# Kernel optimization log

Measured on AMD Instinct MI355X. Metric: run time of the kernel, lower is better.

Reference implementation:

```python
import jax, jax.numpy as jnp
import numpy as np

N, E, NREL = 50000, 800000, 4
IN, EMB, HID, OUT, LVL = 32, 32, 32, 32, 3


def setup_inputs() -> dict:
    key = jax.random.key(0)
    ks = jax.random.split(key, 24)
    f32 = jnp.float32
    inp = {
        'x': jax.random.normal(ks[0], (N, IN), f32),
        'node_feat': jax.random.normal(ks[1], (N, EMB), f32),
        'edge_feat': jax.random.normal(ks[2], (E, EMB), f32),
        'src': jax.random.randint(ks[3], (E,), 0, N, jnp.int32),
        'dst': jax.random.randint(ks[4], (E,), 0, N, jnp.int32),
        'eid': jax.random.randint(ks[5], (E,), 0, NREL, jnp.int32),
        # layer 1 (in_feat=IN)
        'Wr1': jax.random.normal(ks[6], (NREL, IN + 2 * EMB, HID), f32) * 0.1,
        'attn_w1': jax.random.normal(ks[7], (EMB + HID, 1), f32) * 0.1,
        'loop_w1': jax.random.normal(ks[8], (EMB, HID), f32) * 0.1,
        'h_bias1': jax.random.normal(ks[9], (HID,), f32) * 0.1,
        'amrm_W1': jax.random.normal(ks[10], (LVL, HID, HID), f32) * 0.1,
        'amrm_b1': jax.random.normal(ks[11], (LVL, HID), f32) * 0.1,
        'amrm_a1': jax.random.normal(ks[12], (HID, 1), f32) * 0.1,
        # layer 2 (in_feat=HID)
        'Wr2': jax.random.normal(ks[13], (NREL, HID + 2 * EMB, OUT), f32) * 0.1,
        'attn_w2': jax.random.normal(ks[14], (EMB + OUT, 1), f32) * 0.1,
        'loop_w2': jax.random.normal(ks[15], (EMB, OUT), f32) * 0.1,
        'h_bias2': jax.random.normal(ks[16], (OUT,), f32) * 0.1,
        'amrm_W2': jax.random.normal(ks[17], (LVL, OUT, OUT), f32) * 0.1,
        'amrm_b2': jax.random.normal(ks[18], (LVL, OUT), f32) * 0.1,
        'amrm_a2': jax.random.normal(ks[19], (OUT, 1), f32) * 0.1,
    }
    return inp


def _rp_layer(feat, node_feat, src, dst, eid, edge_feat,
              Wr, attn_w, loop_w, h_bias, amrm_W, amrm_b, amrm_a):
    n = node_feat.shape[0]
    ones_e = jnp.ones((src.shape[0],), feat.dtype)
    # symmetric-ish degree norm: feat scaled by out-degree^-1/2
    deg_out = jnp.clip(jax.ops.segment_sum(ones_e, src, num_segments=n), 1.0)
    feat = feat * (deg_out ** -0.5)[:, None]
    # per-edge gather + relation-typed linear (grouped GEMM over NREL types)
    xe = jnp.concatenate([feat[src], edge_feat, node_feat[dst]], axis=1)  # [E, in+2*emb]
    m = jnp.zeros((xe.shape[0], Wr.shape[2]), feat.dtype)
    for r in range(Wr.shape[0]):
        m = m + jnp.where((eid == r)[:, None], xe @ Wr[r], 0.0)
    # edge attention + segment softmax over incoming edges per dst node
    z = jax.nn.leaky_relu(jnp.concatenate([node_feat[dst], m], axis=1) @ attn_w)  # [E,1]
    zmax = jax.ops.segment_max(z, dst, num_segments=n)
    ez = jnp.exp(z - zmax[dst])
    a = ez / jax.ops.segment_sum(ez, dst, num_segments=n)[dst]
    # scatter-sum aggregation
    h = jax.ops.segment_sum(a * m, dst, num_segments=n)
    h = h + node_feat @ loop_w
    deg_in = jnp.clip(jax.ops.segment_sum(ones_e, dst, num_segments=n), 1.0)
    h = h * (deg_in ** -0.5)[:, None] + h_bias
    # adaptive multi-level relation module
    lv = jax.nn.relu(jnp.einsum('nh,lho->nlo', h, amrm_W) + amrm_b[None])  # [N,L,O]
    sc = jax.nn.softmax(jnp.einsum('nlo,o->nl', lv, amrm_a[:, 0]), axis=-1)  # [N,L]
    return jnp.einsum('nl,nlo->no', sc, lv)


def reference(x, node_feat, edge_feat, src, dst, eid,
              Wr1, attn_w1, loop_w1, h_bias1, amrm_W1, amrm_b1, amrm_a1,
              Wr2, attn_w2, loop_w2, h_bias2, amrm_W2, amrm_b2, amrm_a2):
    h = jax.nn.relu(_rp_layer(x, node_feat, src, dst, eid, edge_feat,
                              Wr1, attn_w1, loop_w1, h_bias1, amrm_W1, amrm_b1, amrm_a1))
    h = jax.nn.relu(_rp_layer(h, node_feat, src, dst, eid, edge_feat,
                              Wr2, attn_w2, loop_w2, h_bias2, amrm_W2, amrm_b2, amrm_a2))
    return h
```

## Files before the change

kernel.cpp:

```cpp
#include <hip/hip_runtime.h>

#define NN 50000
#define NE 800000

#define O_DEGIN   0
#define O_DEGOUT  50048
#define O_ROWPTR  100096
#define O_CURSOR  150208
#define O_EINFO   200256
#define O_FEATN   1800256
#define O_ZF      3400256
#define O_ZNRD    3600320
#define O_VV      3800384
#define O_EZ      3800832
#define O_NFT     4600832
#define O_WDENT   6200832
#define O_YACCT   6450880
#define O_H1      19250880
#define O_PACC    20850880


__global__ __launch_bounds__(256) void k_deg(const int* __restrict__ src,
                                             const int* __restrict__ dst,
                                             int* degin, int* degout) {
    int e = blockIdx.x * 256 + threadIdx.x;
    if (e < NE) {
        atomicAdd(&degin[dst[e]], 1);
        atomicAdd(&degout[src[e]], 1);
    }
}

__global__ __launch_bounds__(1024) void k_scan(const int* __restrict__ degin,
                                               int* rowptr, int* cursor) {
    __shared__ int swsum[16];
    __shared__ int stot;
    int t = threadIdx.x;
    int lane = t & 63, w = t >> 6;
    int carry = 0;
    for (int ch = 0; ch < 4; ch++) {
        int base = ch * 16384 + t * 16;
        int v[16];
        int s = 0;
#pragma unroll
        for (int j = 0; j < 16; j++) {
            v[j] = (base + j < NN) ? degin[base + j] : 0;
            s += v[j];
        }
        int incl = s;
#pragma unroll
        for (int off = 1; off < 64; off <<= 1) {
            int x = __shfl_up(incl, off, 64);
            if (lane >= off) incl += x;
        }
        if (lane == 63) swsum[w] = incl;
        __syncthreads();
        if (w == 0) {
            int y = (lane < 16) ? swsum[lane] : 0;
            int yi = y;
#pragma unroll
            for (int off = 1; off < 16; off <<= 1) {
                int x = __shfl_up(yi, off, 64);
                if (lane >= off) yi += x;
            }
            if (lane < 16) swsum[lane] = yi - y;
            if (lane == 15) stot = yi;
        }
        __syncthreads();
        int excl = carry + swsum[w] + (incl - s);
#pragma unroll
        for (int j = 0; j < 16; j++) {
            if (base + j < NN) { rowptr[base + j] = excl; cursor[base + j] = excl; }
            excl += v[j];
        }
        carry += stot;
        __syncthreads();
    }
    if (t == 0) rowptr[NN] = carry;
}

__global__ __launch_bounds__(256) void k_scatter(const int* __restrict__ src,
                                                 const int* __restrict__ dst,
                                                 const int* __restrict__ eid,
                                                 int* cursor, int2* einfo) {
    int e = blockIdx.x * 256 + threadIdx.x;
    if (e >= NE) return;
    int slot = atomicAdd(&cursor[dst[e]], 1);
    einfo[slot] = make_int2(src[e] | (eid[e] << 20), e);
}


__global__ __launch_bounds__(384) void k_prevec(const float* __restrict__ Wr,
                                                const float* __restrict__ attw,
                                                float* __restrict__ vvec) {
    int t = threadIdx.x;
    int r = (t >> 5) & 3, k = t & 31, part = t >> 7;
    int row = (part == 0) ? (32 + k) : (part == 1) ? k : (64 + k);
    const float* wrow = Wr + (size_t)r * 3072 + row * 32;
    float s = 0.f;
#pragma unroll
    for (int c = 0; c < 32; c++) s += wrow[c] * attw[32 + c];
    vvec[t] = s;
}

__global__ __launch_bounds__(128) void k_nodeproj(const float* __restrict__ feat,
                                                  const float* __restrict__ nfeat,
                                                  const float* __restrict__ attw,
                                                  const float* __restrict__ vvec,
                                                  const int* __restrict__ degout,
                                                  float* __restrict__ featn,
                                                  float* __restrict__ nfT,
                                                  float* __restrict__ zF,
                                                  float* __restrict__ znrd) {
    int n = blockIdx.x * 128 + threadIdx.x;
    if (n >= NN) return;
    int dg = degout[n];
    float sc0 = rsqrtf((float)(dg > 1 ? dg : 1));
    const float* fin = feat + (size_t)n * 32;
    const float* nin = nfeat + (size_t)n * 32;
    float fv[32], nv[32];
#pragma unroll
    for (int k = 0; k < 32; k += 4) {
        float4 f4 = *(const float4*)&fin[k];
        fv[k] = f4.x * sc0; fv[k + 1] = f4.y * sc0;
        fv[k + 2] = f4.z * sc0; fv[k + 3] = f4.w * sc0;
        float4 n4 = *(const float4*)&nin[k];
        nv[k] = n4.x; nv[k + 1] = n4.y; nv[k + 2] = n4.z; nv[k + 3] = n4.w;
    }
    float* fo = featn + (size_t)n * 32;
#pragma unroll
    for (int k = 0; k < 32; k += 4)
        *(float4*)&fo[k] = make_float4(fv[k], fv[k + 1], fv[k + 2], fv[k + 3]);
#pragma unroll
    for (int k = 0; k < 32; k++) nfT[(size_t)k * NN + n] = nv[k];
    float zn = 0.f;
#pragma unroll
    for (int k = 0; k < 32; k++) zn += nv[k] * attw[k];
#pragma unroll
    for (int r = 0; r < 4; r++) {
        float zf = 0.f, zd = 0.f;
        const float* vf = vvec + 128 + r * 32;
        const float* vd = vvec + 256 + r * 32;
#pragma unroll
        for (int k = 0; k < 32; k++) { zf += fv[k] * vf[k]; zd += nv[k] * vd[k]; }
        zF[r * NN + n] = zf;
        znrd[r * NN + n] = zn + zd;
    }
}

__global__ __launch_bounds__(256) void k_ez(const int* __restrict__ src,
                                            const int* __restrict__ dst,
                                            const int* __restrict__ eid,
                                            const float* __restrict__ efeat,
                                            const float* __restrict__ zF,
                                            const float* __restrict__ znrd,
                                            const float* __restrict__ vvec,
                                            float* __restrict__ ez) {
    int e = blockIdx.x * 256 + threadIdx.x;
    int s = src[e], d = dst[e], r = eid[e];
    const float* er = efeat + (size_t)e * 32;
    float d0 = 0.f, d1 = 0.f, d2 = 0.f, d3 = 0.f;
#pragma unroll
    for (int k = 0; k < 32; k += 4) {
        float4 f = *(const float4*)&er[k];
        d0 += f.x * vvec[k]       + f.y * vvec[k + 1]
            + f.z * vvec[k + 2]   + f.w * vvec[k + 3];
        d1 += f.x * vvec[32 + k]  + f.y * vvec[33 + k]
            + f.z * vvec[34 + k]  + f.w * vvec[35 + k];
        d2 += f.x * vvec[64 + k]  + f.y * vvec[65 + k]
            + f.z * vvec[66 + k]  + f.w * vvec[67 + k];
        d3 += f.x * vvec[96 + k]  + f.y * vvec[97 + k]
            + f.z * vvec[98 + k]  + f.w * vvec[99 + k];
    }
    float dot = (r == 0) ? d0 : (r == 1) ? d1 : (r == 2) ? d2 : d3;
    float z = znrd[r * NN + d] + zF[r * NN + s] + dot;
    z = z > 0.f ? z : 0.01f * z;
    ez[e] = __expf(z);
}

__global__ __launch_bounds__(512) void k_agg(const int* __restrict__ rowptr,
                                             const int2* __restrict__ einfo,
                                             const float* __restrict__ ez,
                                             const float* __restrict__ efeat,
                                             const float* __restrict__ featn,
                                             float* __restrict__ yaccT,
                                             float* __restrict__ wdenT) {
    __shared__ float sT[256 * 9];
    int tid = threadIdx.x;
    int lane = tid & 63;
    int wid = tid >> 6;
    int n0 = blockIdx.x * 8;
    int n = n0 + wid;
    int c = lane & 31;
    int p = lane >> 5;

    int rp0 = rowptr[n];
    int deg = rowptr[n + 1] - rp0;

    float yf0 = 0.f, yf1 = 0.f, yf2 = 0.f, yf3 = 0.f;
    float ye0 = 0.f, ye1 = 0.f, ye2 = 0.f, ye3 = 0.f;
    float w0 = 0.f, w1 = 0.f, w2 = 0.f, w3 = 0.f, den = 0.f;

    int2 meA = make_int2(0, 0), meB = make_int2(0, 0);
    float ezA = 0.f, efA = 0.f, fnA = 0.f;
    if (p < deg) {
        meA = einfo[rp0 + p];
        ezA = ez[meA.y];
        efA = efeat[(size_t)meA.y * 32 + c];
        fnA = featn[(size_t)(meA.x & 0xFFFFF) * 32 + c];
    }
    if (p + 2 < deg) meB = einfo[rp0 + p + 2];

    for (int t = p; t < deg; t += 2) {
        float ezB = 0.f, efB = 0.f, fnB = 0.f;
        int2 meC = make_int2(0, 0);
        if (t + 2 < deg) {
            ezB = ez[meB.y];
            efB = efeat[(size_t)meB.y * 32 + c];
            fnB = featn[(size_t)(meB.x & 0xFFFFF) * 32 + c];
        }
        if (t + 4 < deg) meC = einfo[rp0 + t + 4];
        int rb = meA.x >> 20;
        float e0 = (rb == 0) ? ezA : 0.f;
        float e1 = (rb == 1) ? ezA : 0.f;
        float e2 = (rb == 2) ? ezA : 0.f;
        float e3 = (rb == 3) ? ezA : 0.f;
        yf0 += e0 * fnA; yf1 += e1 * fnA; yf2 += e2 * fnA; yf3 += e3 * fnA;
        ye0 += e0 * efA; ye1 += e1 * efA; ye2 += e2 * efA; ye3 += e3 * efA;
        w0 += e0; w1 += e1; w2 += e2; w3 += e3;
        den += ezA;
        meA = meB; ezA = ezB; efA = efB; fnA = fnB; meB = meC;
    }

    yf0 += __shfl_xor(yf0, 32); yf1 += __shfl_xor(yf1, 32);
    yf2 += __shfl_xor(yf2, 32); yf3 += __shfl_xor(yf3, 32);
    ye0 += __shfl_xor(ye0, 32); ye1 += __shfl_xor(ye1, 32);
    ye2 += __shfl_xor(ye2, 32); ye3 += __shfl_xor(ye3, 32);
    w0 += __shfl_xor(w0, 32); w1 += __shfl_xor(w1, 32);
    w2 += __shfl_xor(w2, 32); w3 += __shfl_xor(w3, 32);
    den += __shfl_xor(den, 32);

    if (lane < 5) {
        float wv = (lane == 0) ? w0 : (lane == 1) ? w1 : (lane == 2) ? w2
                 : (lane == 3) ? w3 : den;
        wdenT[lane * NN + n] = wv;
    }

    {
        int kb = 128 * p + c;
        sT[(kb +  0) * 9 + wid] = p ? ye0 : yf0;
        sT[(kb + 32) * 9 + wid] = p ? ye1 : yf1;
        sT[(kb + 64) * 9 + wid] = p ? ye2 : yf2;
        sT[(kb + 96) * 9 + wid] = p ? ye3 : yf3;
    }
    __syncthreads();
    int k = tid >> 1, hf = tid & 1;
    float4 v = make_float4(sT[k * 9 + hf * 4 + 0], sT[k * 9 + hf * 4 + 1],
                           sT[k * 9 + hf * 4 + 2], sT[k * 9 + hf * 4 + 3]);
    *(float4*)&yaccT[(size_t)k * NN + n0 + hf * 4] = v;
}

__global__ __launch_bounds__(256) void k_postA(const float* __restrict__ yaccT,
                                               const float* __restrict__ wdenT,
                                               const float* __restrict__ nfT,
                                               const float* __restrict__ Wr,
                                               float* __restrict__ pacc) {
    int n = blockIdx.x * 256 + threadIdx.x;
    if (n >= NN) return;
    int r = blockIdx.y;

    float nv[32];
#pragma unroll
    for (int k = 0; k < 32; k++) nv[k] = nfT[(size_t)k * NN + n];
    float wr = wdenT[r * NN + n];

    const float* W = Wr + (size_t)r * 3072;
    const float* ufc = yaccT + (size_t)(r * 32) * NN + n;
    const float* uec = yaccT + (size_t)(128 + r * 32) * NN + n;

    float acc[32];
#pragma unroll
    for (int i = 0; i < 32; i++) acc[i] = 0.f;
    for (int k4 = 0; k4 < 32; k4 += 4) {
        float a0 = ufc[(size_t)(k4 + 0) * NN], a1 = ufc[(size_t)(k4 + 1) * NN];
        float a2 = ufc[(size_t)(k4 + 2) * NN], a3 = ufc[(size_t)(k4 + 3) * NN];
        float b0 = uec[(size_t)(k4 + 0) * NN], b1 = uec[(size_t)(k4 + 1) * NN];
        float b2 = uec[(size_t)(k4 + 2) * NN], b3 = uec[(size_t)(k4 + 3) * NN];
        float g0 = wr * nv[k4],     g1 = wr * nv[k4 + 1];
        float g2 = wr * nv[k4 + 2], g3 = wr * nv[k4 + 3];
        const float* Wk = W + k4 * 32;
#pragma unroll
        for (int i = 0; i < 32; i++)
            acc[i] += a0 * Wk[i]        + a1 * Wk[32 + i]
                    + a2 * Wk[64 + i]   + a3 * Wk[96 + i]
                    + b0 * Wk[1024 + i] + b1 * Wk[1056 + i]
                    + b2 * Wk[1088 + i] + b3 * Wk[1120 + i]
                    + g0 * Wk[2048 + i] + g1 * Wk[2080 + i]
                    + g2 * Wk[2112 + i] + g3 * Wk[2144 + i];
    }
    float* po = pacc + (size_t)(r * 32) * NN + n;
#pragma unroll
    for (int i = 0; i < 32; i++) po[(size_t)i * NN] = acc[i];
}

__global__ __launch_bounds__(256) void k_postB(const int* __restrict__ rowptr,
                                               const float* __restrict__ pacc,
                                               const float* __restrict__ wdenT,
                                               const float* __restrict__ nfT,
                                               const float* __restrict__ lw,
                                               const float* __restrict__ hbias,
                                               const float* __restrict__ aW,
                                               const float* __restrict__ ab,
                                               const float* __restrict__ aa,
                                               float* __restrict__ out) {
    int n = blockIdx.x * 256 + threadIdx.x;
    if (n >= NN) return;
    int deg = rowptr[n + 1] - rowptr[n];
    float den = wdenT[4 * NN + n];
    float invden = (deg > 0) ? 1.f / den : 0.f;

    float nv[32];
#pragma unroll
    for (int k = 0; k < 32; k++) nv[k] = nfT[(size_t)k * NN + n];

    float h[32];
#pragma unroll
    for (int i = 0; i < 32; i++) {
        float s = pacc[(size_t)i * NN + n]
                + pacc[(size_t)(32 + i) * NN + n]
                + pacc[(size_t)(64 + i) * NN + n]
                + pacc[(size_t)(96 + i) * NN + n];
        h[i] = s * invden;
    }
    for (int k4 = 0; k4 < 32; k4 += 4) {
        const float* Lk = lw + k4 * 32;
#pragma unroll
        for (int i = 0; i < 32; i++)
            h[i] += nv[k4] * Lk[i] + nv[k4 + 1] * Lk[32 + i]
                  + nv[k4 + 2] * Lk[64 + i] + nv[k4 + 3] * Lk[96 + i];
    }
    float hsc = rsqrtf((float)(deg > 1 ? deg : 1));
#pragma unroll
    for (int i = 0; i < 32; i++) h[i] = h[i] * hsc + hbias[i];

    float acc[32];
    float s[3];
#pragma unroll
    for (int l = 0; l < 3; l++) {
        const float* A = aW + (size_t)l * 1024;
#pragma unroll
        for (int i = 0; i < 32; i++) acc[i] = ab[l * 32 + i];
        for (int k4 = 0; k4 < 32; k4 += 4) {
            const float* Ak = A + k4 * 32;
#pragma unroll
            for (int i = 0; i < 32; i++)
                acc[i] += h[k4] * Ak[i] + h[k4 + 1] * Ak[32 + i]
                        + h[k4 + 2] * Ak[64 + i] + h[k4 + 3] * Ak[96 + i];
        }
        float sl = 0.f;
#pragma unroll
        for (int i = 0; i < 32; i++) {
            float lv = acc[i] > 0.f ? acc[i] : 0.f;
            sl += lv * aa[i];
        }
        s[l] = sl;
    }
    float mx = fmaxf(s[0], fmaxf(s[1], s[2]));
    float e0 = __expf(s[0] - mx), e1 = __expf(s[1] - mx), e2 = __expf(s[2] - mx);
    float inv = 1.f / (e0 + e1 + e2);
    float scl[3] = {e0 * inv, e1 * inv, e2 * inv};

    float outv[32];
#pragma unroll
    for (int i = 0; i < 32; i++) outv[i] = 0.f;
#pragma unroll
    for (int l = 0; l < 3; l++) {
        const float* A = aW + (size_t)l * 1024;
#pragma unroll
        for (int i = 0; i < 32; i++) acc[i] = ab[l * 32 + i];
        for (int k4 = 0; k4 < 32; k4 += 4) {
            const float* Ak = A + k4 * 32;
#pragma unroll
            for (int i = 0; i < 32; i++)
                acc[i] += h[k4] * Ak[i] + h[k4 + 1] * Ak[32 + i]
                        + h[k4 + 2] * Ak[64 + i] + h[k4 + 3] * Ak[96 + i];
        }
#pragma unroll
        for (int i = 0; i < 32; i++) {
            float lv = acc[i] > 0.f ? acc[i] : 0.f;
            outv[i] += scl[l] * lv;
        }
    }
    float* op = out + (size_t)n * 32;
#pragma unroll
    for (int i = 0; i < 32; i += 4)
        *(float4*)&op[i] = make_float4(fmaxf(outv[i], 0.f), fmaxf(outv[i + 1], 0.f),
                                       fmaxf(outv[i + 2], 0.f), fmaxf(outv[i + 3], 0.f));
}


static void launch_layer(const float* feat, const float* nf, const float* efeat,
                         const int* src, const int* dst, const int* eid,
                         const float* Wr, const float* attw, const float* lw,
                         const float* hb, const float* aW, const float* ab,
                         const float* aa, float* wsf, int* wsi, float* out,
                         hipStream_t stream) {
    k_prevec<<<1, 384, 0, stream>>>(Wr, attw, wsf + O_VV);
    k_nodeproj<<<391, 128, 0, stream>>>(feat, nf, attw, wsf + O_VV, wsi + O_DEGOUT,
                                        wsf + O_FEATN, wsf + O_NFT,
                                        wsf + O_ZF, wsf + O_ZNRD);
    k_ez<<<3125, 256, 0, stream>>>(src, dst, eid, efeat, wsf + O_ZF, wsf + O_ZNRD,
                                   wsf + O_VV, wsf + O_EZ);
    k_agg<<<6250, 512, 0, stream>>>(wsi + O_ROWPTR, (const int2*)(wsi + O_EINFO),
                                    wsf + O_EZ, efeat, wsf + O_FEATN,
                                    wsf + O_YACCT, wsf + O_WDENT);
    k_postA<<<dim3(196, 4), 256, 0, stream>>>(wsf + O_YACCT, wsf + O_WDENT,
                                              wsf + O_NFT, Wr, wsf + O_PACC);
    k_postB<<<196, 256, 0, stream>>>(wsi + O_ROWPTR, wsf + O_PACC, wsf + O_WDENT,
                                     wsf + O_NFT, lw, hb, aW, ab, aa, out);
}

extern "C" void kernel_launch(void* const* d_in, const int* in_sizes, int n_in,
                              void* d_out, int out_size, void* d_ws, size_t ws_size,
                              hipStream_t stream) {
    const float* x     = (const float*)d_in[0];
    const float* nfeat = (const float*)d_in[1];
    const float* efeat = (const float*)d_in[2];
    const int*   src   = (const int*)d_in[3];
    const int*   dst   = (const int*)d_in[4];
    const int*   eid   = (const int*)d_in[5];
    const float* Wr1   = (const float*)d_in[6];
    const float* attw1 = (const float*)d_in[7];
    const float* lw1   = (const float*)d_in[8];
    const float* hb1   = (const float*)d_in[9];
    const float* aW1   = (const float*)d_in[10];
    const float* ab1   = (const float*)d_in[11];
    const float* aa1   = (const float*)d_in[12];
    const float* Wr2   = (const float*)d_in[13];
    const float* attw2 = (const float*)d_in[14];
    const float* lw2   = (const float*)d_in[15];
    const float* hb2   = (const float*)d_in[16];
    const float* aW2   = (const float*)d_in[17];
    const float* ab2   = (const float*)d_in[18];
    const float* aa2   = (const float*)d_in[19];

    float* wsf = (float*)d_ws;
    int*   wsi = (int*)d_ws;
    float* out = (float*)d_out;

    hipMemsetAsync(d_ws, 0, (size_t)O_ROWPTR * 4, stream);

    k_deg<<<NE / 256, 256, 0, stream>>>(src, dst, wsi + O_DEGIN, wsi + O_DEGOUT);
    k_scan<<<1, 1024, 0, stream>>>(wsi + O_DEGIN, wsi + O_ROWPTR, wsi + O_CURSOR);
    k_scatter<<<NE / 256, 256, 0, stream>>>(src, dst, eid, wsi + O_CURSOR,
                                            (int2*)(wsi + O_EINFO));

    launch_layer(x, nfeat, efeat, src, dst, eid, Wr1, attw1, lw1, hb1, aW1, ab1, aa1,
                 wsf, wsi, wsf + O_H1, stream);
    launch_layer(wsf + O_H1, nfeat, efeat, src, dst, eid, Wr2, attw2, lw2, hb2,
                 aW2, ab2, aa2, wsf, wsi, out, stream);
}
```

Before: 700.8 us.

## Fuse relation-typed projection into edge aggregation kernel, drop transposed intermediates

Fuses the per-relation Wr projection (formerly k_postA) into the aggregation kernel. Each warp now multiplies its per-node accumulated sums by Wr from shared memory, and writes a node-major 32-wide result plus the softmax denominator. The edge loop now handles 4 edges in parallel per wave with float2 loads instead of 2 edges with scalar loads. This removes the large transposed yaccT/pacc round-trips through global memory and one kernel launch. The cost is extra per-block arithmetic and repeated Wr reads from cache in the aggregation kernel.

```diff
diff --git a/kernel.cpp b/kernel.cpp
--- a/kernel.cpp
+++ b/kernel.cpp
@@ -18,6 +18,7 @@
 #define O_YACCT   6450880
 #define O_H1      19250880
 #define O_PACC    20850880
+#define O_HACC    O_PACC
 
 
 __global__ __launch_bounds__(256) void k_deg(const int* __restrict__ src,
@@ -177,134 +178,119 @@
     ez[e] = __expf(z);
 }
 
-__global__ __launch_bounds__(512) void k_agg(const int* __restrict__ rowptr,
-                                             const int2* __restrict__ einfo,
-                                             const float* __restrict__ ez,
-                                             const float* __restrict__ efeat,
-                                             const float* __restrict__ featn,
-                                             float* __restrict__ yaccT,
-                                             float* __restrict__ wdenT) {
-    __shared__ float sT[256 * 9];
+#define R2(v) { v += __shfl_xor(v, 16); v += __shfl_xor(v, 32); }
+__global__ __launch_bounds__(512) void k_aggf(const int* __restrict__ rowptr,
+                                              const int2* __restrict__ einfo,
+                                              const float* __restrict__ ez,
+                                              const float* __restrict__ efeat,
+                                              const float* __restrict__ featn,
+                                              const float* __restrict__ nfeat,
+                                              const float* __restrict__ Wr,
+                                              float* __restrict__ hacc,
+                                              float* __restrict__ wden) {
+    __shared__ alignas(16) float sT[8 * 256];
+    __shared__ alignas(16) float snv[8 * 32];
+    __shared__ float sw[8 * 4];
     int tid = threadIdx.x;
     int lane = tid & 63;
     int wid = tid >> 6;
-    int n0 = blockIdx.x * 8;
-    int n = n0 + wid;
-    int c = lane & 31;
-    int p = lane >> 5;
+    int n = blockIdx.x * 8 + wid;
+    int g = lane >> 4;
+    int c2 = lane & 15;
+
+    if (lane < 32) snv[wid * 32 + lane] = nfeat[(size_t)n * 32 + lane];
 
     int rp0 = rowptr[n];
     int deg = rowptr[n + 1] - rp0;
 
-    float yf0 = 0.f, yf1 = 0.f, yf2 = 0.f, yf3 = 0.f;
-    float ye0 = 0.f, ye1 = 0.f, ye2 = 0.f, ye3 = 0.f;
+    float2 yf0 = {0.f, 0.f}, yf1 = {0.f, 0.f}, yf2 = {0.f, 0.f}, yf3 = {0.f, 0.f};
+    float2 ye0 = {0.f, 0.f}, ye1 = {0.f, 0.f}, ye2 = {0.f, 0.f}, ye3 = {0.f, 0.f};
     float w0 = 0.f, w1 = 0.f, w2 = 0.f, w3 = 0.f, den = 0.f;
 
     int2 meA = make_int2(0, 0), meB = make_int2(0, 0);
-    float ezA = 0.f, efA = 0.f, fnA = 0.f;
-    if (p < deg) {
-        meA = einfo[rp0 + p];
+    float ezA = 0.f; float2 efA = {0.f, 0.f}, fnA = {0.f, 0.f};
+    if (g < deg) {
+        meA = einfo[rp0 + g];
         ezA = ez[meA.y];
-        efA = efeat[(size_t)meA.y * 32 + c];
-        fnA = featn[(size_t)(meA.x & 0xFFFFF) * 32 + c];
-    }
-    if (p + 2 < deg) meB = einfo[rp0 + p + 2];
-
-    for (int t = p; t < deg; t += 2) {
-        float ezB = 0.f, efB = 0.f, fnB = 0.f;
+        efA = *(const float2*)&efeat[(size_t)meA.y * 32 + c2 * 2];
+        fnA = *(const float2*)&featn[(size_t)(meA.x & 0xFFFFF) * 32 + c2 * 2];
+    }
+    if (g + 4 < deg) meB = einfo[rp0 + g + 4];
+
+    for (int t = g; t < deg; t += 4) {
+        float ezB = 0.f; float2 efB = {0.f, 0.f}, fnB = {0.f, 0.f};
         int2 meC = make_int2(0, 0);
-        if (t + 2 < deg) {
+        if (t + 4 < deg) {
             ezB = ez[meB.y];
-            efB = efeat[(size_t)meB.y * 32 + c];
-            fnB = featn[(size_t)(meB.x & 0xFFFFF) * 32 + c];
-        }
-        if (t + 4 < deg) meC = einfo[rp0 + t + 4];
+            efB = *(const float2*)&efeat[(size_t)meB.y * 32 + c2 * 2];
+            fnB = *(const float2*)&featn[(size_t)(meB.x & 0xFFFFF) * 32 + c2 * 2];
+        }
+        if (t + 8 < deg) meC = einfo[rp0 + t + 8];
         int rb = meA.x >> 20;
         float e0 = (rb == 0) ? ezA : 0.f;
         float e1 = (rb == 1) ? ezA : 0.f;
         float e2 = (rb == 2) ? ezA : 0.f;
         float e3 = (rb == 3) ? ezA : 0.f;
-        yf0 += e0 * fnA; yf1 += e1 * fnA; yf2 += e2 * fnA; yf3 += e3 * fnA;
-        ye0 += e0 * efA; ye1 += e1 * efA; ye2 += e2 * efA; ye3 += e3 * efA;
+        yf0.x += e0 * fnA.x; yf0.y += e0 * fnA.y;
+        yf1.x += e1 * fnA.x; yf1.y += e1 * fnA.y;
+        yf2.x += e2 * fnA.x; yf2.y += e2 * fnA.y;
+        yf3.x += e3 * fnA.x; yf3.y += e3 * fnA.y;
+        ye0.x += e0 * efA.x; ye0.y += e0 * efA.y;
+        ye1.x += e1 * efA.x; ye1.y += e1 * efA.y;
+        ye2.x += e2 * efA.x; ye2.y += e2 * efA.y;
+        ye3.x += e3 * efA.x; ye3.y += e3 * efA.y;
         w0 += e0; w1 += e1; w2 += e2; w3 += e3;
         den += ezA;
         meA = meB; ezA = ezB; efA = efB; fnA = fnB; meB = meC;
     }
 
-    yf0 += __shfl_xor(yf0, 32); yf1 += __shfl_xor(yf1, 32);
-    yf2 += __shfl_xor(yf2, 32); yf3 += __shfl_xor(yf3, 32);
-    ye0 += __shfl_xor(ye0, 32); ye1 += __shfl_xor(ye1, 32);
-    ye2 += __shfl_xor(ye2, 32); ye3 += __shfl_xor(ye3, 32);
-    w0 += __shfl_xor(w0, 32); w1 += __shfl_xor(w1, 32);
-    w2 += __shfl_xor(w2, 32); w3 += __shfl_xor(w3, 32);
-    den += __shfl_xor(den, 32);
-
-    if (lane < 5) {
-        float wv = (lane == 0) ? w0 : (lane == 1) ? w1 : (lane == 2) ? w2
-                 : (lane == 3) ? w3 : den;
-        wdenT[lane * NN + n] = wv;
-    }
-
-    {
-        int kb = 128 * p + c;
-        sT[(kb +  0) * 9 + wid] = p ? ye0 : yf0;
-        sT[(kb + 32) * 9 + wid] = p ? ye1 : yf1;
-        sT[(kb + 64) * 9 + wid] = p ? ye2 : yf2;
-        sT[(kb + 96) * 9 + wid] = p ? ye3 : yf3;
-    }
-    __syncthreads();
-    int k = tid >> 1, hf = tid & 1;
-    float4 v = make_float4(sT[k * 9 + hf * 4 + 0], sT[k * 9 + hf * 4 + 1],
-                           sT[k * 9 + hf * 4 + 2], sT[k * 9 + hf * 4 + 3]);
-    *(float4*)&yaccT[(size_t)k * NN + n0 + hf * 4] = v;
-}
-
-__global__ __launch_bounds__(256) void k_postA(const float* __restrict__ yaccT,
-                                               const float* __restrict__ wdenT,
-                                               const float* __restrict__ nfT,
-                                               const float* __restrict__ Wr,
-                                               float* __restrict__ pacc) {
-    int n = blockIdx.x * 256 + threadIdx.x;
-    if (n >= NN) return;
-    int r = blockIdx.y;
-
-    float nv[32];
-#pragma unroll
-    for (int k = 0; k < 32; k++) nv[k] = nfT[(size_t)k * NN + n];
-    float wr = wdenT[r * NN + n];
-
-    const float* W = Wr + (size_t)r * 3072;
-    const float* ufc = yaccT + (size_t)(r * 32) * NN + n;
-    const float* uec = yaccT + (size_t)(128 + r * 32) * NN + n;
-
-    float acc[32];
-#pragma unroll
-    for (int i = 0; i < 32; i++) acc[i] = 0.f;
-    for (int k4 = 0; k4 < 32; k4 += 4) {
-        float a0 = ufc[(size_t)(k4 + 0) * NN], a1 = ufc[(size_t)(k4 + 1) * NN];
-        float a2 = ufc[(size_t)(k4 + 2) * NN], a3 = ufc[(size_t)(k4 + 3) * NN];
-        float b0 = uec[(size_t)(k4 + 0) * NN], b1 = uec[(size_t)(k4 + 1) * NN];
-        float b2 = uec[(size_t)(k4 + 2) * NN], b3 = uec[(size_t)(k4 + 3) * NN];
-        float g0 = wr * nv[k4],     g1 = wr * nv[k4 + 1];
-        float g2 = wr * nv[k4 + 2], g3 = wr * nv[k4 + 3];
-        const float* Wk = W + k4 * 32;
-#pragma unroll
-        for (int i = 0; i < 32; i++)
-            acc[i] += a0 * Wk[i]        + a1 * Wk[32 + i]
-                    + a2 * Wk[64 + i]   + a3 * Wk[96 + i]
-                    + b0 * Wk[1024 + i] + b1 * Wk[1056 + i]
-                    + b2 * Wk[1088 + i] + b3 * Wk[1120 + i]
-                    + g0 * Wk[2048 + i] + g1 * Wk[2080 + i]
-                    + g2 * Wk[2112 + i] + g3 * Wk[2144 + i];
-    }
-    float* po = pacc + (size_t)(r * 32) * NN + n;
-#pragma unroll
-    for (int i = 0; i < 32; i++) po[(size_t)i * NN] = acc[i];
+    R2(yf0.x) R2(yf0.y) R2(yf1.x) R2(yf1.y)
+    R2(yf2.x) R2(yf2.y) R2(yf3.x) R2(yf3.y)
+    R2(ye0.x) R2(ye0.y) R2(ye1.x) R2(ye1.y)
+    R2(ye2.x) R2(ye2.y) R2(ye3.x) R2(ye3.y)
+    R2(w0) R2(w1) R2(w2) R2(w3) R2(den)
+
+    float2 pf = (g == 0) ? yf0 : (g == 1) ? yf1 : (g == 2) ? yf2 : yf3;
+    float2 pe = (g == 0) ? ye0 : (g == 1) ? ye1 : (g == 2) ? ye2 : ye3;
+    *(float2*)&sT[wid * 256 + g * 32 + c2 * 2] = pf;
+    *(float2*)&sT[wid * 256 + 128 + g * 32 + c2 * 2] = pe;
+    if (lane < 4)
+        sw[wid * 4 + lane] = (lane == 0) ? w0 : (lane == 1) ? w1
+                           : (lane == 2) ? w2 : w3;
+    if (lane == 0) wden[n] = den;
+
+    int i = lane & 31, half = lane >> 5;
+    float acc = 0.f;
+    const float* sTn = sT + wid * 256 + half * 128;
+    const float* Wb = Wr + (size_t)(half * 32) * 32 + i;
+#pragma unroll
+    for (int kq = 0; kq < 128; kq += 4) {
+        int r = kq >> 5, c = kq & 31;
+        float4 v = *(const float4*)&sTn[kq];
+        const float* wp = Wb + (size_t)r * 3072 + c * 32;
+        acc += v.x * wp[0] + v.y * wp[32] + v.z * wp[64] + v.w * wp[96];
+    }
+#pragma unroll
+    for (int rr = 0; rr < 2; rr++) {
+        int r = half * 2 + rr;
+        float wr = sw[wid * 4 + r];
+        const float* wd = Wr + (size_t)r * 3072 + 2048 + i;
+#pragma unroll
+        for (int c = 0; c < 32; c += 4) {
+            float4 nvq = *(const float4*)&snv[wid * 32 + c];
+            acc += wr * (nvq.x * wd[(size_t)c * 32]
+                       + nvq.y * wd[(size_t)(c + 1) * 32]
+                       + nvq.z * wd[(size_t)(c + 2) * 32]
+                       + nvq.w * wd[(size_t)(c + 3) * 32]);
+        }
+    }
+    acc += __shfl_xor(acc, 32);
+    if (lane < 32) hacc[(size_t)n * 32 + i] = acc;
 }
 
 __global__ __launch_bounds__(256) void k_postB(const int* __restrict__ rowptr,
-                                               const float* __restrict__ pacc,
-                                               const float* __restrict__ wdenT,
+                                               const float* __restrict__ hacc,
+                                               const float* __restrict__ wden,
                                                const float* __restrict__ nfT,
                                                const float* __restrict__ lw,
                                                const float* __restrict__ hbias,
@@ -315,21 +301,19 @@
     int n = blockIdx.x * 256 + threadIdx.x;
     if (n >= NN) return;
     int deg = rowptr[n + 1] - rowptr[n];
-    float den = wdenT[4 * NN + n];
-    float invden = (deg > 0) ? 1.f / den : 0.f;
+    float invden = (deg > 0) ? 1.f / wden[n] : 0.f;
 
     float nv[32];
 #pragma unroll
     for (int k = 0; k < 32; k++) nv[k] = nfT[(size_t)k * NN + n];
 
     float h[32];
-#pragma unroll
-    for (int i = 0; i < 32; i++) {
-        float s = pacc[(size_t)i * NN + n]
-                + pacc[(size_t)(32 + i) * NN + n]
-                + pacc[(size_t)(64 + i) * NN + n]
-                + pacc[(size_t)(96 + i) * NN + n];
-        h[i] = s * invden;
+    const float* hp = hacc + (size_t)n * 32;
+#pragma unroll
+    for (int i = 0; i < 32; i += 4) {
+        float4 v = *(const float4*)&hp[i];
+        h[i] = v.x * invden; h[i + 1] = v.y * invden;
+        h[i + 2] = v.z * invden; h[i + 3] = v.w * invden;
     }
     for (int k4 = 0; k4 < 32; k4 += 4) {
         const float* Lk = lw + k4 * 32;
@@ -410,12 +394,10 @@
                                         wsf + O_ZF, wsf + O_ZNRD);
     k_ez<<<3125, 256, 0, stream>>>(src, dst, eid, efeat, wsf + O_ZF, wsf + O_ZNRD,
                                    wsf + O_VV, wsf + O_EZ);
-    k_agg<<<6250, 512, 0, stream>>>(wsi + O_ROWPTR, (const int2*)(wsi + O_EINFO),
-                                    wsf + O_EZ, efeat, wsf + O_FEATN,
-                                    wsf + O_YACCT, wsf + O_WDENT);
-    k_postA<<<dim3(196, 4), 256, 0, stream>>>(wsf + O_YACCT, wsf + O_WDENT,
-                                              wsf + O_NFT, Wr, wsf + O_PACC);
-    k_postB<<<196, 256, 0, stream>>>(wsi + O_ROWPTR, wsf + O_PACC, wsf + O_WDENT,
+    k_aggf<<<6250, 512, 0, stream>>>(wsi + O_ROWPTR, (const int2*)(wsi + O_EINFO),
+                                     wsf + O_EZ, efeat, wsf + O_FEATN, nf, Wr,
+                                     wsf + O_HACC, wsf + O_WDENT);
+    k_postB<<<196, 256, 0, stream>>>(wsi + O_ROWPTR, wsf + O_HACC, wsf + O_WDENT,
                                      wsf + O_NFT, lw, hb, aW, ab, aa, out);
 }
 
```

Measured after the change: 742.0 us. 1.06x slower.

## Fuse post-aggregation GEMMs into one node-per-half-wave kernel with row-major accumulators

Applied to the files above, without the earlier changes.

k_agg now writes its per-node aggregated accumulators row-major and skips the shared-memory transpose. The two post kernels (per-relation projection into pacc, then loop/AMRM) are merged into one kernel. Each 32-lane half-wave handles one node, staging its accumulator row and node features in LDS, and computes each output channel per lane. This drops the pacc round trip and one launch and replaces the 32-accumulator register-heavy threads with per-lane dot products, uses shuffles for the attention score reduction, and reads untransposed node features directly. Weights are now read per lane with strided global loads, which may cost more cache traffic.

```diff
diff --git a/kernel.cpp b/kernel.cpp
--- a/kernel.cpp
+++ b/kernel.cpp
@@ -15,9 +15,8 @@
 #define O_EZ      3800832
 #define O_NFT     4600832
 #define O_WDENT   6200832
-#define O_YACCT   6450880
+#define O_YACC    6450880
 #define O_H1      19250880
-#define O_PACC    20850880
 
 
 __global__ __launch_bounds__(256) void k_deg(const int* __restrict__ src,
@@ -182,9 +181,8 @@
                                              const float* __restrict__ ez,
                                              const float* __restrict__ efeat,
                                              const float* __restrict__ featn,
-                                             float* __restrict__ yaccT,
+                                             float* __restrict__ yacc,
                                              float* __restrict__ wdenT) {
-    __shared__ float sT[256 * 9];
     int tid = threadIdx.x;
     int lane = tid & 63;
     int wid = tid >> 6;
@@ -245,156 +243,115 @@
         wdenT[lane * NN + n] = wv;
     }
 
+    float* yr = yacc + (size_t)n * 256 + p * 128 + c;
+    yr[0]  = p ? ye0 : yf0;
+    yr[32] = p ? ye1 : yf1;
+    yr[64] = p ? ye2 : yf2;
+    yr[96] = p ? ye3 : yf3;
+}
+
+__global__ __launch_bounds__(256) void k_postAB(const int* __restrict__ rowptr,
+                                                const float* __restrict__ yacc,
+                                                const float* __restrict__ wdenT,
+                                                const float* __restrict__ nfeat,
+                                                const float* __restrict__ Wr,
+                                                const float* __restrict__ lw,
+                                                const float* __restrict__ hbias,
+                                                const float* __restrict__ aW,
+                                                const float* __restrict__ ab,
+                                                const float* __restrict__ aa,
+                                                float* __restrict__ out) {
+    __shared__ alignas(16) float sy[8 * 256];
+    __shared__ alignas(16) float snf[8 * 32];
+    __shared__ float sh[8 * 32];
+    int tid = threadIdx.x;
+    int n0 = blockIdx.x * 8;
+
     {
-        int kb = 128 * p + c;
-        sT[(kb +  0) * 9 + wid] = p ? ye0 : yf0;
-        sT[(kb + 32) * 9 + wid] = p ? ye1 : yf1;
-        sT[(kb + 64) * 9 + wid] = p ? ye2 : yf2;
-        sT[(kb + 96) * 9 + wid] = p ? ye3 : yf3;
+        const float4* ys = (const float4*)(yacc + (size_t)n0 * 256);
+        float4* yd = (float4*)sy;
+        yd[tid] = ys[tid];
+        yd[tid + 256] = ys[tid + 256];
+        snf[tid] = nfeat[(size_t)n0 * 32 + tid];
     }
     __syncthreads();
-    int k = tid >> 1, hf = tid & 1;
-    float4 v = make_float4(sT[k * 9 + hf * 4 + 0], sT[k * 9 + hf * 4 + 1],
-                           sT[k * 9 + hf * 4 + 2], sT[k * 9 + hf * 4 + 3]);
-    *(float4*)&yaccT[(size_t)k * NN + n0 + hf * 4] = v;
-}
-
-__global__ __launch_bounds__(256) void k_postA(const float* __restrict__ yaccT,
-                                               const float* __restrict__ wdenT,
-                                               const float* __restrict__ nfT,
-                                               const float* __restrict__ Wr,
-                                               float* __restrict__ pacc) {
-    int n = blockIdx.x * 256 + threadIdx.x;
-    if (n >= NN) return;
-    int r = blockIdx.y;
-
-    float nv[32];
-#pragma unroll
-    for (int k = 0; k < 32; k++) nv[k] = nfT[(size_t)k * NN + n];
-    float wr = wdenT[r * NN + n];
-
-    const float* W = Wr + (size_t)r * 3072;
-    const float* ufc = yaccT + (size_t)(r * 32) * NN + n;
-    const float* uec = yaccT + (size_t)(128 + r * 32) * NN + n;
-
-    float acc[32];
-#pragma unroll
-    for (int i = 0; i < 32; i++) acc[i] = 0.f;
-    for (int k4 = 0; k4 < 32; k4 += 4) {
-        float a0 = ufc[(size_t)(k4 + 0) * NN], a1 = ufc[(size_t)(k4 + 1) * NN];
-        float a2 = ufc[(size_t)(k4 + 2) * NN], a3 = ufc[(size_t)(k4 + 3) * NN];
-        float b0 = uec[(size_t)(k4 + 0) * NN], b1 = uec[(size_t)(k4 + 1) * NN];
-        float b2 = uec[(size_t)(k4 + 2) * NN], b3 = uec[(size_t)(k4 + 3) * NN];
-        float g0 = wr * nv[k4],     g1 = wr * nv[k4 + 1];
-        float g2 = wr * nv[k4 + 2], g3 = wr * nv[k4 + 3];
-        const float* Wk = W + k4 * 32;
-#pragma unroll
-        for (int i = 0; i < 32; i++)
-            acc[i] += a0 * Wk[i]        + a1 * Wk[32 + i]
-                    + a2 * Wk[64 + i]   + a3 * Wk[96 + i]
-                    + b0 * Wk[1024 + i] + b1 * Wk[1056 + i]
-                    + b2 * Wk[1088 + i] + b3 * Wk[1120 + i]
-                    + g0 * Wk[2048 + i] + g1 * Wk[2080 + i]
-                    + g2 * Wk[2112 + i] + g3 * Wk[2144 + i];
-    }
-    float* po = pacc + (size_t)(r * 32) * NN + n;
-#pragma unroll
-    for (int i = 0; i < 32; i++) po[(size_t)i * NN] = acc[i];
-}
-
-__global__ __launch_bounds__(256) void k_postB(const int* __restrict__ rowptr,
-                                               const float* __restrict__ pacc,
-                                               const float* __restrict__ wdenT,
-                                               const float* __restrict__ nfT,
-                                               const float* __restrict__ lw,
-                                               const float* __restrict__ hbias,
-                                               const float* __restrict__ aW,
-                                               const float* __restrict__ ab,
-                                               const float* __restrict__ aa,
-                                               float* __restrict__ out) {
-    int n = blockIdx.x * 256 + threadIdx.x;
-    if (n >= NN) return;
+
+    int lane = tid & 63;
+    int wid = tid >> 6;
+    int g = lane >> 5, i = lane & 31;
+    int node = wid * 2 + g;
+    int n = n0 + node;
     int deg = rowptr[n + 1] - rowptr[n];
-    float den = wdenT[4 * NN + n];
-    float invden = (deg > 0) ? 1.f / den : 0.f;
-
-    float nv[32];
-#pragma unroll
-    for (int k = 0; k < 32; k++) nv[k] = nfT[(size_t)k * NN + n];
-
-    float h[32];
-#pragma unroll
-    for (int i = 0; i < 32; i++) {
-        float s = pacc[(size_t)i * NN + n]
-                + pacc[(size_t)(32 + i) * NN + n]
-                + pacc[(size_t)(64 + i) * NN + n]
-                + pacc[(size_t)(96 + i) * NN + n];
-        h[i] = s * invden;
-    }
-    for (int k4 = 0; k4 < 32; k4 += 4) {
-        const float* Lk = lw + k4 * 32;
-#pragma unroll
-        for (int i = 0; i < 32; i++)
-            h[i] += nv[k4] * Lk[i] + nv[k4 + 1] * Lk[32 + i]
-                  + nv[k4 + 2] * Lk[64 + i] + nv[k4 + 3] * Lk[96 + i];
+    const float* row = sy + node * 256;
+    const float* nv = snf + node * 32;
+
+    float h = 0.f;
+#pragma unroll
+    for (int part = 0; part < 2; part++) {
+#pragma unroll
+        for (int r = 0; r < 4; r++) {
+            const float* W = Wr + (size_t)r * 3072 + (part ? 1024 : 0) + i;
+            const float* rw = row + part * 128 + r * 32;
+#pragma unroll
+            for (int c = 0; c < 32; c += 4) {
+                float4 v = *(const float4*)&rw[c];
+                h += v.x * W[(size_t)c * 32] + v.y * W[(size_t)(c + 1) * 32]
+                   + v.z * W[(size_t)(c + 2) * 32] + v.w * W[(size_t)(c + 3) * 32];
+            }
+        }
+    }
+#pragma unroll
+    for (int r = 0; r < 4; r++) {
+        float wr = wdenT[(size_t)r * NN + n];
+        const float* W = Wr + (size_t)r * 3072 + 2048 + i;
+        float t = 0.f;
+#pragma unroll
+        for (int c = 0; c < 32; c += 4) {
+            float4 v = *(const float4*)&nv[c];
+            t += v.x * W[(size_t)c * 32] + v.y * W[(size_t)(c + 1) * 32]
+               + v.z * W[(size_t)(c + 2) * 32] + v.w * W[(size_t)(c + 3) * 32];
+        }
+        h += wr * t;
+    }
+    float den = wdenT[(size_t)4 * NN + n];
+    h *= (deg > 0) ? 1.f / den : 0.f;
+    {
+        const float* L = lw + i;
+#pragma unroll
+        for (int c = 0; c < 32; c += 4) {
+            float4 v = *(const float4*)&nv[c];
+            h += v.x * L[(size_t)c * 32] + v.y * L[(size_t)(c + 1) * 32]
+               + v.z * L[(size_t)(c + 2) * 32] + v.w * L[(size_t)(c + 3) * 32];
+        }
     }
     float hsc = rsqrtf((float)(deg > 1 ? deg : 1));
-#pragma unroll
-    for (int i = 0; i < 32; i++) h[i] = h[i] * hsc + hbias[i];
-
-    float acc[32];
-    float s[3];
+    h = h * hsc + hbias[i];
+    sh[node * 32 + i] = h;
+
+    float lv[3], s[3];
+    const float* hn = sh + node * 32;
 #pragma unroll
     for (int l = 0; l < 3; l++) {
-        const float* A = aW + (size_t)l * 1024;
-#pragma unroll
-        for (int i = 0; i < 32; i++) acc[i] = ab[l * 32 + i];
-        for (int k4 = 0; k4 < 32; k4 += 4) {
-            const float* Ak = A + k4 * 32;
-#pragma unroll
-            for (int i = 0; i < 32; i++)
-                acc[i] += h[k4] * Ak[i] + h[k4 + 1] * Ak[32 + i]
-                        + h[k4 + 2] * Ak[64 + i] + h[k4 + 3] * Ak[96 + i];
-        }
-        float sl = 0.f;
-#pragma unroll
-        for (int i = 0; i < 32; i++) {
-            float lv = acc[i] > 0.f ? acc[i] : 0.f;
-            sl += lv * aa[i];
-        }
-        s[l] = sl;
+        float a = ab[l * 32 + i];
+        const float* A = aW + (size_t)l * 1024 + i;
+#pragma unroll
+        for (int c = 0; c < 32; c += 4) {
+            float4 v = *(const float4*)&hn[c];
+            a += v.x * A[(size_t)c * 32] + v.y * A[(size_t)(c + 1) * 32]
+               + v.z * A[(size_t)(c + 2) * 32] + v.w * A[(size_t)(c + 3) * 32];
+        }
+        lv[l] = a > 0.f ? a : 0.f;
+        float t = lv[l] * aa[i];
+        t += __shfl_xor(t, 16); t += __shfl_xor(t, 8);
+        t += __shfl_xor(t, 4);  t += __shfl_xor(t, 2);
+        t += __shfl_xor(t, 1);
+        s[l] = t;
     }
     float mx = fmaxf(s[0], fmaxf(s[1], s[2]));
     float e0 = __expf(s[0] - mx), e1 = __expf(s[1] - mx), e2 = __expf(s[2] - mx);
     float inv = 1.f / (e0 + e1 + e2);
-    float scl[3] = {e0 * inv, e1 * inv, e2 * inv};
-
-    float outv[32];
-#pragma unroll
-    for (int i = 0; i < 32; i++) outv[i] = 0.f;
-#pragma unroll
-    for (int l = 0; l < 3; l++) {
-        const float* A = aW + (size_t)l * 1024;
-#pragma unroll
-        for (int i = 0; i < 32; i++) acc[i] = ab[l * 32 + i];
-        for (int k4 = 0; k4 < 32; k4 += 4) {
-            const float* Ak = A + k4 * 32;
-#pragma unroll
-            for (int i = 0; i < 32; i++)
-                acc[i] += h[k4] * Ak[i] + h[k4 + 1] * Ak[32 + i]
-                        + h[k4 + 2] * Ak[64 + i] + h[k4 + 3] * Ak[96 + i];
-        }
-#pragma unroll
-        for (int i = 0; i < 32; i++) {
-            float lv = acc[i] > 0.f ? acc[i] : 0.f;
-            outv[i] += scl[l] * lv;
-        }
-    }
-    float* op = out + (size_t)n * 32;
-#pragma unroll
-    for (int i = 0; i < 32; i += 4)
-        *(float4*)&op[i] = make_float4(fmaxf(outv[i], 0.f), fmaxf(outv[i + 1], 0.f),
-                                       fmaxf(outv[i + 2], 0.f), fmaxf(outv[i + 3], 0.f));
+    float o = (e0 * lv[0] + e1 * lv[1] + e2 * lv[2]) * inv;
+    out[(size_t)n * 32 + i] = fmaxf(o, 0.f);
 }
 
 
@@ -412,11 +369,9 @@
                                    wsf + O_VV, wsf + O_EZ);
     k_agg<<<6250, 512, 0, stream>>>(wsi + O_ROWPTR, (const int2*)(wsi + O_EINFO),
                                     wsf + O_EZ, efeat, wsf + O_FEATN,
-                                    wsf + O_YACCT, wsf + O_WDENT);
-    k_postA<<<dim3(196, 4), 256, 0, stream>>>(wsf + O_YACCT, wsf + O_WDENT,
-                                              wsf + O_NFT, Wr, wsf + O_PACC);
-    k_postB<<<196, 256, 0, stream>>>(wsi + O_ROWPTR, wsf + O_PACC, wsf + O_WDENT,
-                                     wsf + O_NFT, lw, hb, aW, ab, aa, out);
+                                    wsf + O_YACC, wsf + O_WDENT);
+    k_postAB<<<6250, 256, 0, stream>>>(wsi + O_ROWPTR, wsf + O_YACC, wsf + O_WDENT,
+                                       nf, Wr, lw, hb, aW, ab, aa, out);
 }
 
 extern "C" void kernel_launch(void* const* d_in, const int* in_sizes, int n_in,
```

After: 2.642 ms. 3.77x slower.
